# Optimization experiments

Measured on AMD Instinct MI355X. Metric: run time of the kernel, lower is better.

Reference implementation:

```python
import jax, jax.numpy as jnp
import numpy as np

BITS = 4
MAXQ = 15          # (1 << BITS) - 1
PACK = 32 // BITS  # 8 values packed per int32


def dequantize(qweight, qzeros, scales, g_idx):
    """GPTQ 4-bit dequant. qweight: [K//8, N] int32, qzeros: [G, N//8] int32,
    scales: [G, N] float, g_idx: [K] int32 -> dense W [K, N] float."""
    N = qweight.shape[1]
    shifts = (jnp.arange(PACK, dtype=jnp.uint32) * BITS)  # [8]
    qw = qweight.astype(jnp.uint32)
    # unpack along K: k = row*8 + j  (matches shifter = (k % 8) * bits)
    w_int = ((qw[:, None, :] >> shifts[None, :, None]) & MAXQ).reshape(-1, N)  # [K, N]
    qz = qzeros.astype(jnp.uint32)
    # unpack along N: n = col*8 + j  (matches zeros_shifter = (n % 8) * bits)
    z_int = ((qz[:, :, None] >> shifts[None, None, :]) & MAXQ).reshape(qzeros.shape[0], -1) + 1  # [G, N]
    dt = scales.dtype
    # group-wise dequant: w = (q - zero) * scale, gathered per-row via g_idx
    return (w_int.astype(dt) - z_int[g_idx].astype(dt)) * scales[g_idx]


def setup_inputs() -> dict:
    key = jax.random.key(0)
    k1, k2, k3, k4, k5 = jax.random.split(key, 5)
    M, K, N, GS = 128, 4096, 11008, 128
    G = K // GS
    x = jax.random.normal(k1, (M, K), dtype=jnp.float32)
    qweight = jax.random.randint(k2, (K // PACK, N), 0, 2147483647, dtype=jnp.int32)
    qzeros = jax.random.randint(k3, (G, N // PACK), 0, 2147483647, dtype=jnp.int32)
    scales = jax.random.uniform(k4, (G, N), dtype=jnp.float32, minval=0.001, maxval=0.01)
    bias = jax.random.normal(k5, (N,), dtype=jnp.float32)
    g_idx = (jnp.arange(K, dtype=jnp.int32) // GS).astype(jnp.int32)
    return {"x": x, "qweight": qweight, "qzeros": qzeros, "scales": scales,
            "bias": bias, "g_idx": g_idx}


def reference(x, qweight, qzeros, scales, bias, g_idx):
    w = dequantize(qweight, qzeros, scales, g_idx)  # [K, N]
    return x @ w + bias
```

## Files before the change

### kernel.cpp

```cpp
#include <hip/hip_runtime.h>
#include <stdint.h>


#define M_DIM 128
#define K_DIM 4096
#define N_DIM 11008
#define GS    128
#define NG    32
#define SPLIT 4
#define GPB   (NG / SPLIT)
#define PART_STRIDE ((size_t)M_DIM * N_DIM)

typedef _Float16 half8  __attribute__((ext_vector_type(8)));
typedef _Float16 half2t __attribute__((ext_vector_type(2)));
typedef _Float16 half4t __attribute__((ext_vector_type(4)));
typedef float    f32x4  __attribute__((ext_vector_type(4)));

__global__ void k_prep(const float* __restrict__ x, const int* __restrict__ qzeros,
                       const float* __restrict__ scales,
                       _Float16* __restrict__ xh, float* __restrict__ zs) {
    int b = blockIdx.x, tid = threadIdx.x;
    if (b < 512) {
        int i = (b * 256 + tid) * 4;
        float4 v = *(const float4*)(x + i);
        half4t o;
        o[0] = (_Float16)v.x; o[1] = (_Float16)v.y;
        o[2] = (_Float16)v.z; o[3] = (_Float16)v.w;
        *(half4t*)(xh + i) = o;
    } else {
        b -= 512;
        int g = b / 43;
        int n = (b - g * 43) * 256 + tid;
        unsigned qz = (unsigned)qzeros[g * (N_DIM / 8) + (n >> 3)];
        float z = (float)((qz >> ((n & 7) * 4)) & 15u) + 1.0f;
        zs[g * N_DIM + n] = z * scales[g * N_DIM + n];
    }
}

__device__ __forceinline__ void load_lds16(const void* g, void* l) {
    __builtin_amdgcn_global_load_lds(
        (const __attribute__((address_space(1))) unsigned int*)g,
        (__attribute__((address_space(3))) unsigned int*)l, 16, 0, 0);
}

__device__ __forceinline__ half8 dequant8(unsigned q, half2t S2, half2t Z2) {
    const half2t BIAS = __builtin_bit_cast(half2t, 0x64006400u);
    half2t w[4];
#pragma unroll
    for (int p = 0; p < 4; ++p) {
        unsigned r = __builtin_amdgcn_perm(q, q, 0x00010001u * (unsigned)p);
        unsigned t = (r & 0x00F0000Fu) | 0x64006400u;
        w[p] = __builtin_elementwise_fma(__builtin_bit_cast(half2t, t) - BIAS, S2, Z2);
    }
    half4t lo = __builtin_shufflevector(w[0], w[1], 0, 1, 2, 3);
    half4t hi = __builtin_shufflevector(w[2], w[3], 0, 1, 2, 3);
    return __builtin_shufflevector(lo, hi, 0, 1, 2, 3, 4, 5, 6, 7);
}

__global__ __launch_bounds__(512, 4)
void k_gemm(const _Float16* __restrict__ xh,
            const int*      __restrict__ qweight,
            const float*    __restrict__ scales,
            const float*    __restrict__ zst,
            float*          __restrict__ part)
{
    __shared__ _Float16 As[2][128 * 128];

    const int tid  = threadIdx.x;
    const int lane = tid & 63;
    const int w    = tid >> 6;
    const int wy   = w >> 1;
    const int wx   = w & 1;
    const int q    = lane >> 4;
    const int lr   = lane & 15;

    const int n0 = blockIdx.x * 64;
    const int g0 = blockIdx.y * GPB;
    int ncol[2] = { n0 + wx * 32 + lr, n0 + wx * 32 + lr + 16 };

    f32x4 acc[2][2];
#pragma unroll
    for (int f = 0; f < 2; ++f)
#pragma unroll
        for (int h = 0; h < 2; ++h)
            acc[f][h] = (f32x4){0.f, 0.f, 0.f, 0.f};

    int cm[4], ckb[4];
#pragma unroll
    for (int it = 0; it < 4; ++it) {
        int c = it * 512 + tid;
        cm[it]  = c >> 4;
        ckb[it] = (c & 15) ^ (cm[it] & 15);
    }
    const int wave_lds = w * 64 * 8;

#pragma unroll
    for (int it = 0; it < 4; ++it)
        load_lds16(xh + (size_t)cm[it] * K_DIM + g0 * GS + ckb[it] * 8,
                   &As[0][it * 512 * 8 + wave_lds]);
    unsigned qwn[8];
    float scn[2], zcn[2];
#pragma unroll
    for (int kk = 0; kk < 4; ++kk)
#pragma unroll
        for (int h = 0; h < 2; ++h)
            qwn[kk * 2 + h] = (unsigned)qweight[(size_t)(g0 * 16 + kk * 4 + q) * N_DIM + ncol[h]];
#pragma unroll
    for (int h = 0; h < 2; ++h) {
        scn[h] = scales[(size_t)g0 * N_DIM + ncol[h]];
        zcn[h] = zst[(size_t)g0 * N_DIM + ncol[h]];
    }

    int p = 0;
    for (int g = 0; g < GPB; ++g) {
        unsigned qw[8];
        float sc[2], zc[2];
#pragma unroll
        for (int i = 0; i < 8; ++i) qw[i] = qwn[i];
#pragma unroll
        for (int h = 0; h < 2; ++h) { sc[h] = scn[h]; zc[h] = zcn[h]; }

        __syncthreads();

        if (g + 1 < GPB) {
            int gn = g0 + g + 1;
#pragma unroll
            for (int it = 0; it < 4; ++it)
                load_lds16(xh + (size_t)cm[it] * K_DIM + gn * GS + ckb[it] * 8,
                           &As[p ^ 1][it * 512 * 8 + wave_lds]);
#pragma unroll
            for (int kk = 0; kk < 4; ++kk)
#pragma unroll
                for (int h = 0; h < 2; ++h)
                    qwn[kk * 2 + h] = (unsigned)qweight[(size_t)(gn * 16 + kk * 4 + q) * N_DIM + ncol[h]];
#pragma unroll
            for (int h = 0; h < 2; ++h) {
                scn[h] = scales[(size_t)gn * N_DIM + ncol[h]];
                zcn[h] = zst[(size_t)gn * N_DIM + ncol[h]];
            }
        }

        half2t S2[2], Z2[2];
#pragma unroll
        for (int h = 0; h < 2; ++h) {
            float s = sc[h], z1 = zc[h];
            S2[h][0] = (_Float16)s;
            S2[h][1] = (_Float16)(s * 0.0625f);
            Z2[h][0] = (_Float16)(-z1);
            Z2[h][1] = (_Float16)(-z1);
        }

#pragma unroll
        for (int kk = 0; kk < 4; ++kk) {
            half8 bf[2];
#pragma unroll
            for (int h = 0; h < 2; ++h)
                bf[h] = dequant8(qw[kk * 2 + h], S2[h], Z2[h]);
#pragma unroll
            for (int f = 0; f < 2; ++f) {
                int m   = wy * 32 + f * 16 + lr;
                int kb2 = (kk * 4 + q) ^ lr;
                half8 af = *(const half8*)(&As[p][m * 128 + kb2 * 8]);
#pragma unroll
                for (int h = 0; h < 2; ++h)
                    acc[f][h] = __builtin_amdgcn_mfma_f32_16x16x32_f16(af, bf[h], acc[f][h], 0, 0, 0);
            }
        }
        p ^= 1;
    }

    float* po = part + (size_t)blockIdx.y * PART_STRIDE;
#pragma unroll
    for (int f = 0; f < 2; ++f) {
        int mrow = wy * 32 + f * 16 + q * 4;
#pragma unroll
        for (int h = 0; h < 2; ++h)
#pragma unroll
            for (int r = 0; r < 4; ++r)
                po[(size_t)(mrow + r) * N_DIM + ncol[h]] = acc[f][h][r];
    }
}

__global__ void k_reduce(const float* __restrict__ part, const float* __restrict__ bias,
                         float* __restrict__ out) {
    int i = (blockIdx.x * 256 + threadIdx.x) * 4;
    int m = i / N_DIM;
    int n = i - m * N_DIM;
    f32x4 s = *(const f32x4*)(bias + n);
#pragma unroll
    for (int sp = 0; sp < SPLIT; ++sp)
        s += *(const f32x4*)(part + sp * PART_STRIDE + i);
    *(f32x4*)(out + i) = s;
}

extern "C" void kernel_launch(void* const* d_in, const int* in_sizes, int n_in,
                              void* d_out, int out_size, void* d_ws, size_t ws_size,
                              hipStream_t stream) {
    const float* x       = (const float*)d_in[0];
    const int*   qweight = (const int*)d_in[1];
    const int*   qzeros  = (const int*)d_in[2];
    const float* scales  = (const float*)d_in[3];
    const float* bias    = (const float*)d_in[4];

    char* ws = (char*)d_ws;
    _Float16* xh   = (_Float16*)ws;
    float*    zst  = (float*)(ws + 1048576);
    float*    part = (float*)(ws + 1048576 + 1409024);

    k_prep  <<<dim3(1888),            dim3(256), 0, stream>>>(x, qzeros, scales, xh, zst);
    k_gemm  <<<dim3(N_DIM/64, SPLIT), dim3(512), 0, stream>>>(xh, qweight, scales, zst, part);
    k_reduce<<<dim3(1376),            dim3(256), 0, stream>>>(part, bias, (float*)d_out);
}
```

Before: 107.9 us.

## Split K across wave pairs in GEMM block, reduce partial accumulators via LDS

```diff
diff --git a/kernel.cpp b/kernel.cpp
--- a/kernel.cpp
+++ b/kernel.cpp
@@ -69,8 +69,9 @@
     const int tid  = threadIdx.x;
     const int lane = tid & 63;
     const int w    = tid >> 6;
-    const int wy   = w >> 1;
     const int wx   = w & 1;
+    const int wy   = (w >> 1) & 1;
+    const int kh   = w >> 2;
     const int q    = lane >> 4;
     const int lr   = lane & 15;
 
@@ -78,9 +79,9 @@
     const int g0 = blockIdx.y * GPB;
     int ncol[2] = { n0 + wx * 32 + lr, n0 + wx * 32 + lr + 16 };
 
-    f32x4 acc[2][2];
-#pragma unroll
-    for (int f = 0; f < 2; ++f)
+    f32x4 acc[4][2];
+#pragma unroll
+    for (int f = 0; f < 4; ++f)
 #pragma unroll
         for (int h = 0; h < 2; ++h)
             acc[f][h] = (f32x4){0.f, 0.f, 0.f, 0.f};
@@ -98,13 +99,13 @@
     for (int it = 0; it < 4; ++it)
         load_lds16(xh + (size_t)cm[it] * K_DIM + g0 * GS + ckb[it] * 8,
                    &As[0][it * 512 * 8 + wave_lds]);
-    unsigned qwn[8];
+    unsigned qwn[4];
     float scn[2], zcn[2];
 #pragma unroll
-    for (int kk = 0; kk < 4; ++kk)
+    for (int t = 0; t < 2; ++t)
 #pragma unroll
         for (int h = 0; h < 2; ++h)
-            qwn[kk * 2 + h] = (unsigned)qweight[(size_t)(g0 * 16 + kk * 4 + q) * N_DIM + ncol[h]];
+            qwn[t * 2 + h] = (unsigned)qweight[(size_t)(g0 * 16 + (kh * 2 + t) * 4 + q) * N_DIM + ncol[h]];
 #pragma unroll
     for (int h = 0; h < 2; ++h) {
         scn[h] = scales[(size_t)g0 * N_DIM + ncol[h]];
@@ -113,10 +114,10 @@
 
     int p = 0;
     for (int g = 0; g < GPB; ++g) {
-        unsigned qw[8];
+        unsigned qw[4];
         float sc[2], zc[2];
 #pragma unroll
-        for (int i = 0; i < 8; ++i) qw[i] = qwn[i];
+        for (int i = 0; i < 4; ++i) qw[i] = qwn[i];
 #pragma unroll
         for (int h = 0; h < 2; ++h) { sc[h] = scn[h]; zc[h] = zcn[h]; }
 
@@ -129,10 +130,10 @@
                 load_lds16(xh + (size_t)cm[it] * K_DIM + gn * GS + ckb[it] * 8,
                            &As[p ^ 1][it * 512 * 8 + wave_lds]);
 #pragma unroll
-            for (int kk = 0; kk < 4; ++kk)
+            for (int t = 0; t < 2; ++t)
 #pragma unroll
                 for (int h = 0; h < 2; ++h)
-                    qwn[kk * 2 + h] = (unsigned)qweight[(size_t)(gn * 16 + kk * 4 + q) * N_DIM + ncol[h]];
+                    qwn[t * 2 + h] = (unsigned)qweight[(size_t)(gn * 16 + (kh * 2 + t) * 4 + q) * N_DIM + ncol[h]];
 #pragma unroll
             for (int h = 0; h < 2; ++h) {
                 scn[h] = scales[(size_t)gn * N_DIM + ncol[h]];
@@ -151,14 +152,15 @@
         }
 
 #pragma unroll
-        for (int kk = 0; kk < 4; ++kk) {
+        for (int t = 0; t < 2; ++t) {
+            const int kk = kh * 2 + t;
             half8 bf[2];
 #pragma unroll
             for (int h = 0; h < 2; ++h)
-                bf[h] = dequant8(qw[kk * 2 + h], S2[h], Z2[h]);
-#pragma unroll
-            for (int f = 0; f < 2; ++f) {
-                int m   = wy * 32 + f * 16 + lr;
+                bf[h] = dequant8(qw[t * 2 + h], S2[h], Z2[h]);
+#pragma unroll
+            for (int f = 0; f < 4; ++f) {
+                int m   = wy * 64 + f * 16 + lr;
                 int kb2 = (kk * 4 + q) ^ lr;
                 half8 af = *(const half8*)(&As[p][m * 128 + kb2 * 8]);
 #pragma unroll
@@ -169,15 +171,30 @@
         p ^= 1;
     }
 
-    float* po = part + (size_t)blockIdx.y * PART_STRIDE;
-#pragma unroll
-    for (int f = 0; f < 2; ++f) {
-        int mrow = wy * 32 + f * 16 + q * 4;
-#pragma unroll
-        for (int h = 0; h < 2; ++h)
-#pragma unroll
-            for (int r = 0; r < 4; ++r)
-                po[(size_t)(mrow + r) * N_DIM + ncol[h]] = acc[f][h][r];
+    __syncthreads();
+    float* red = (float*)&As[0][0];
+    const int pid = w & 3;
+    if (w >= 4) {
+#pragma unroll
+        for (int f = 0; f < 4; ++f)
+#pragma unroll
+            for (int h = 0; h < 2; ++h)
+                *(f32x4*)(red + pid * 2048 + (f * 2 + h) * 256 + lane * 4) = acc[f][h];
+    }
+    __syncthreads();
+    if (w < 4) {
+        float* po = part + (size_t)blockIdx.y * PART_STRIDE;
+#pragma unroll
+        for (int f = 0; f < 4; ++f) {
+            int mrow = wy * 64 + f * 16 + q * 4;
+#pragma unroll
+            for (int h = 0; h < 2; ++h) {
+                f32x4 o = acc[f][h] + *(const f32x4*)(red + pid * 2048 + (f * 2 + h) * 256 + lane * 4);
+#pragma unroll
+                for (int r = 0; r < 4; ++r)
+                    po[(size_t)(mrow + r) * N_DIM + ncol[h]] = o[r];
+            }
+        }
     }
 }
 
```

Result: faster. 103.6 us (-4.0%).
